# Kernel optimization log

Hardware: AMD Instinct MI355X
Metric: run time of the kernel (lower is better)

The kernel has to match this reference:

```python
import jax, jax.numpy as jnp
import numpy as np

DIM = 320; HEADS = 8; DHEAD = 40; CTX_DIM = 768
INNER = HEADS * DHEAD; FF_INNER = 4 * DIM
B = 1; N = 4096; M = 77
SCALE = DHEAD ** -0.5


def setup_inputs() -> dict:
    key = jax.random.key(0)
    ks = jax.random.split(key, 16)
    p = lambda i, shape: jax.random.normal(ks[i], shape, dtype=jnp.float32) * 0.02
    return {
        "x": jax.random.normal(ks[0], (B, N, DIM), dtype=jnp.float32),
        "context": jax.random.normal(ks[1], (B, M, CTX_DIM), dtype=jnp.float32),
        "focused_attention_mask": jax.random.uniform(ks[2], (1, M, M), dtype=jnp.float32),
        "g1": jnp.ones((DIM,), jnp.float32), "b1": jnp.zeros((DIM,), jnp.float32),
        "g2": jnp.ones((DIM,), jnp.float32), "b2": jnp.zeros((DIM,), jnp.float32),
        "g3": jnp.ones((DIM,), jnp.float32), "b3": jnp.zeros((DIM,), jnp.float32),
        "Wq1": p(3, (DIM, INNER)), "Wk1": p(4, (DIM, INNER)), "Wv1": p(5, (DIM, INNER)),
        "Wo1": p(6, (INNER, DIM)), "bo1": jnp.zeros((DIM,), jnp.float32),
        "Wq2": p(7, (DIM, INNER)), "Wk2": p(8, (CTX_DIM, INNER)), "Wv2": p(9, (CTX_DIM, INNER)),
        "Wo2": p(10, (INNER, DIM)), "bo2": jnp.zeros((DIM,), jnp.float32),
        "Wff1": p(11, (DIM, 2 * FF_INNER)), "bff1": jnp.zeros((2 * FF_INNER,), jnp.float32),
        "Wff2": p(12, (FF_INNER, DIM)), "bff2": jnp.zeros((DIM,), jnp.float32),
        "use_fca": 1,
    }


def _ln(x, g, b):
    mu = x.mean(-1, keepdims=True)
    var = jnp.mean((x - mu) ** 2, -1, keepdims=True)
    return (x - mu) * jax.lax.rsqrt(var + 1e-5) * g + b


def _attn(xn, ctx, Wq, Wk, Wv, Wo, bo, fam, use_fca):
    b, n, _ = xn.shape
    heads = lambda t: t.reshape(b, t.shape[1], HEADS, DHEAD).transpose(0, 2, 1, 3)  # b h n d
    q, k, v = heads(xn @ Wq), heads(ctx @ Wk), heads(ctx @ Wv)
    sim = jnp.einsum('bhid,bhjd->bhij', q, k) * SCALE
    if use_fca:
        m = fam.shape[-1]  # fam: [1, m, m], batch must be 1 (repeat_interleave semantics)
        fw = jnp.einsum('bhqk,dk->bhqd', sim[..., :m], fam[0])
        fw = jnp.minimum(jnp.abs(fw), 1.0)
        fw = fw / (jnp.max(fw, axis=-1, keepdims=True) + 1e-6)
        fw = (fw > 0.6).astype(sim.dtype)
        sim = sim.at[..., :m].add((fw - 1.0) * 50.0)
    a = jax.nn.softmax(sim, axis=-1)
    o = jnp.einsum('bhij,bhjd->bhid', a, v).transpose(0, 2, 1, 3).reshape(b, n, INNER)
    return o @ Wo + bo


def reference(x, context, focused_attention_mask,
              g1, b1, g2, b2, g3, b3,
              Wq1, Wk1, Wv1, Wo1, bo1,
              Wq2, Wk2, Wv2, Wo2, bo2,
              Wff1, bff1, Wff2, bff2, use_fca):
    # attn1: self-attention (context=None in original -> use_fca forced to 0)
    h1 = _ln(x, g1, b1)
    x = _attn(h1, h1, Wq1, Wk1, Wv1, Wo1, bo1, None, 0) + x
    # attn2: cross-attention with focused-attention mask
    h2 = _ln(x, g2, b2)
    x = _attn(h2, context, Wq2, Wk2, Wv2, Wo2, bo2, focused_attention_mask, int(use_fca)) + x
    # GEGLU feed-forward
    h3 = _ln(x, g3, b3)
    proj = h3 @ Wff1 + bff1
    a_, gate = jnp.split(proj, 2, axis=-1)
    x = (a_ * jax.nn.gelu(gate, approximate=False)) @ Wff2 + bff2 + x
    return x
```

## Files before the change

kernel.cpp:

```cpp
#include <hip/hip_runtime.h>
#include <math.h>

typedef __bf16 bf16_t;
typedef __bf16 bf16x8 __attribute__((ext_vector_type(8)));
typedef __bf16 bf16x4 __attribute__((ext_vector_type(4)));
typedef float  f32x4  __attribute__((ext_vector_type(4)));
typedef _Float16 f16_t;
typedef _Float16 f16x4 __attribute__((ext_vector_type(4)));
typedef _Float16 f16x8 __attribute__((ext_vector_type(8)));
typedef __fp16 hf16x2 __attribute__((ext_vector_type(2)));

static constexpr float ATT_SCALE = 0.15811388300841897f;
static constexpr float SC2 = 0.22811031f;
static constexpr float LOG2E = 1.4426950408889634f;

__device__ __forceinline__ bf16_t f2b(float f) {
  unsigned u = __float_as_uint(f);
  u = (u + 0x7fffu + ((u >> 16) & 1u)) >> 16;
  unsigned short s = (unsigned short)u;
  bf16_t r;
  *(unsigned short*)&r = s;
  return r;
}
__device__ __forceinline__ float b2f(bf16_t b) {
  unsigned short s = *(const unsigned short*)&b;
  return __uint_as_float(((unsigned)s) << 16);
}
__device__ __forceinline__ void sto(float v, float* p)  { *p = v; }
__device__ __forceinline__ void sto(float v, bf16_t* p) { *p = f2b(v); }
__device__ __forceinline__ unsigned pkh2(float a, float b) {
  hf16x2 h = __builtin_amdgcn_cvt_pkrtz(a, b);
  return *(unsigned*)&h;
}

__global__ __launch_bounds__(256) void prep_kernel(
    const float* __restrict__ Wq1, const float* __restrict__ Wk1, const float* __restrict__ Wv1,
    const float* __restrict__ Wo1, const float* __restrict__ Wq2,
    const float* __restrict__ Wk2, const float* __restrict__ Wv2, const float* __restrict__ Wo2,
    const float* __restrict__ Wff1, const float* __restrict__ Wff2,
    const float* __restrict__ fam,
    bf16_t* __restrict__ wqkvt, bf16_t* __restrict__ wo1t, float* __restrict__ wkv2t,
    bf16_t* __restrict__ wo2t, bf16_t* __restrict__ wff1t, bf16_t* __restrict__ wff2t,
    bf16_t* __restrict__ wq2th, bf16_t* __restrict__ wq2tl,
    bf16_t* __restrict__ famh, bf16_t* __restrict__ faml)
{
  const int T1 = 960*320;
  const int T2 = T1 + 320*320;
  const int T3 = T2 + 768*640;
  const int T4 = T3 + 320*320;
  const int T5 = T4 + 2560*320;
  const int T6 = T5 + 320*1280;
  const int T7 = T6 + 320*320;
  const int T8 = T7 + 96*96;
  for (int i = blockIdx.x*256 + threadIdx.x; i < T8; i += gridDim.x*256) {
    if (i < T1) {
      int n = i / 320, k = i - n*320;
      float v = (n < 320) ? Wq1[k*320+n] * SC2
              : (n < 640) ? Wk1[k*320+n-320] : Wv1[k*320+n-640];
      wqkvt[i] = f2b(v);
    } else if (i < T2) {
      int e = i - T1; int n = e / 320, k = e - n*320;
      wo1t[e] = f2b(Wo1[k*320+n]);
    } else if (i < T3) {
      int e = i - T2; int n = e / 768, k = e - n*768;
      wkv2t[e] = (n < 320) ? Wk2[k*320+n] : Wv2[k*320+n-320];
    } else if (i < T4) {
      int e = i - T3; int n = e / 320, k = e - n*320;
      wo2t[e] = f2b(Wo2[k*320+n]);
    } else if (i < T5) {
      int e = i - T4; int n = e / 320, k = e - n*320;
      wff1t[e] = f2b(Wff1[(size_t)k*2560+n]);
    } else if (i < T6) {
      int e = i - T5; int n = e / 1280, k = e - n*1280;
      wff2t[e] = f2b(Wff2[k*320+n]);
    } else if (i < T7) {
      int e = i - T6; int n = e / 320, k = e - n*320;
      float v = Wq2[k*320+n];
      bf16_t h = f2b(v);
      wq2th[e] = h;
      wq2tl[e] = f2b(v - b2f(h));
    } else {
      int e = i - T7; int d = e / 96, k = e - d*96;
      float v = (d < 77 && k < 77) ? fam[d*77 + k] : 0.f;
      bf16_t h = f2b(v);
      famh[e] = h;
      faml[e] = f2b(v - b2f(h));
    }
  }
}

template<typename OT>
__global__ __launch_bounds__(256) void ln_kernel(
    const float* __restrict__ x, const float* __restrict__ g, const float* __restrict__ b,
    OT* __restrict__ out)
{
  const int lane = threadIdx.x & 63;
  const int row = blockIdx.x * 4 + (threadIdx.x >> 6);
  const float* xr = x + (size_t)row * 320;
  float v[5], s = 0.f, s2 = 0.f;
#pragma unroll
  for (int i = 0; i < 5; i++) { v[i] = xr[lane + i*64]; s += v[i]; s2 += v[i]*v[i]; }
#pragma unroll
  for (int o = 32; o; o >>= 1) { s += __shfl_xor(s, o); s2 += __shfl_xor(s2, o); }
  float mu = s * (1.f/320.f);
  float rs = rsqrtf(fmaxf(s2*(1.f/320.f) - mu*mu, 0.f) + 1e-5f);
#pragma unroll
  for (int i = 0; i < 5; i++) {
    int c = lane + i*64;
    sto((v[i]-mu)*rs*g[c] + b[c], &out[(size_t)row*320 + c]);
  }
}

__global__ __launch_bounds__(256) void ln2_split_kernel(
    const float* __restrict__ x, const float* __restrict__ g, const float* __restrict__ b,
    bf16_t* __restrict__ hi, bf16_t* __restrict__ lo)
{
  const int lane = threadIdx.x & 63;
  const int row = blockIdx.x * 4 + (threadIdx.x >> 6);
  const float* xr = x + (size_t)row * 320;
  float v[5], s = 0.f, s2 = 0.f;
#pragma unroll
  for (int i = 0; i < 5; i++) { v[i] = xr[lane + i*64]; s += v[i]; s2 += v[i]*v[i]; }
#pragma unroll
  for (int o = 32; o; o >>= 1) { s += __shfl_xor(s, o); s2 += __shfl_xor(s2, o); }
  float mu = s * (1.f/320.f);
  float rs = rsqrtf(fmaxf(s2*(1.f/320.f) - mu*mu, 0.f) + 1e-5f);
#pragma unroll
  for (int i = 0; i < 5; i++) {
    int c = lane + i*64;
    float y = (v[i]-mu)*rs*g[c] + b[c];
    bf16_t h = f2b(y);
    hi[(size_t)row*320 + c] = h;
    lo[(size_t)row*320 + c] = f2b(y - b2f(h));
  }
}

__global__ __launch_bounds__(256) void kv2_dot_kernel(
    const float* __restrict__ ctx, const float* __restrict__ wkv2t, float* __restrict__ kv2)
{
  const int gid = blockIdx.x*16 + (threadIdx.x >> 4);
  const int q = threadIdx.x & 15;
  const int m = gid / 640, n = gid - m*640;
  const float4* a = (const float4*)(ctx + (size_t)m*768);
  const float4* b = (const float4*)(wkv2t + (size_t)n*768);
  float acc = 0.f;
#pragma unroll
  for (int i = 0; i < 12; i++) {
    float4 av = a[i*16+q], bv = b[i*16+q];
    acc += av.x*bv.x + av.y*bv.y + av.z*bv.z + av.w*bv.w;
  }
#pragma unroll
  for (int o = 8; o; o >>= 1) acc += __shfl_xor(acc, o);
  if (q == 0) kv2[(size_t)m*640 + n] = acc;
}

__global__ __launch_bounds__(256) void kv2_post_kernel(
    const float* __restrict__ kv2, bf16_t* __restrict__ k2h, bf16_t* __restrict__ k2l,
    bf16_t* __restrict__ v2t)
{
  const int NK = 8*96*64;
  const int NV = 8*48*96;
  int i = blockIdx.x*256 + threadIdx.x;
  if (i < NK) {
    int h = i / (96*64), r = i - h*96*64, j = r >> 6, d = r & 63;
    float v = (j < 77 && d < 40) ? kv2[(size_t)j*640 + h*40 + d] : 0.f;
    bf16_t hh = f2b(v);
    k2h[i] = hh;
    k2l[i] = f2b(v - b2f(hh));
  } else if (i < NK + NV) {
    int e = i - NK;
    int h = e / (48*96), r = e - h*48*96, d = r / 96, j = r - d*96;
    v2t[e] = f2b((d < 40 && j < 77) ? kv2[(size_t)j*640 + 320 + h*40 + d] : 0.f);
  }
}

__global__ __launch_bounds__(256) void repack_vt_kernel(
    const bf16_t* __restrict__ qkvb, f16_t* __restrict__ vpack, bf16_t* __restrict__ kpack)
{
  __shared__ f16_t T[64*44];
  const int tid = threadIdx.x;
  const int t0 = blockIdx.x * 64, h = blockIdx.y;
  for (int e = tid; e < 320; e += 256) {
    int t = e / 5, c8 = (e - t*5) * 8;
    bf16x8 v = *(const bf16x8*)(qkvb + (size_t)(t0+t)*960 + 640 + h*40 + c8);
    f16_t* dst = &T[t*44 + c8];
#pragma unroll
    for (int j = 0; j < 8; j++) dst[j] = (f16_t)b2f(v[j]);
  }
  __syncthreads();
  for (int e = tid; e < 3072; e += 256) {
    int dt = e >> 10;
    int r  = e & 1023;
    int g2 = r >> 9, o = r & 511;
    int lane = o >> 3, j = o & 7;
    int qd = lane >> 4, ln = lane & 15;
    int d = dt*16 + ln;
    int key = g2*32 + ((j & 4) ? 16 : 0) + qd*4 + (j & 3);
    float val;
    if (d < 40)       val = (float)T[key*44 + d];
    else if (d == 40) val = 1.0f;
    else              val = 0.0f;
    vpack[(((size_t)h*3 + dt)*128 + (t0 >> 5) + g2)*512 + o] = (f16_t)val;
  }
  for (int e = tid; e < 2560; e += 256) {
    int g = e / 640, o = e - g*640;
    int key = t0 + g*16;
    bf16_t val;
    if (o < 512) {
      int lane = o >> 3, j = o & 7;
      int qd = lane >> 4, ln = lane & 15;
      val = qkvb[(size_t)(key + ln)*960 + 320 + h*40 + qd*8 + j];
    } else {
      int o2 = o - 512; int ln = o2 >> 3, j = o2 & 7;
      val = qkvb[(size_t)(key + ln)*960 + 320 + h*40 + 32 + j];
    }
    kpack[((size_t)h*256 + (t0 >> 4) + g)*640 + o] = val;
  }
}

__global__ __launch_bounds__(256, 4) void flash_self_kernel(
    const bf16_t* __restrict__ qkvb, const bf16_t* __restrict__ kpack,
    const f16_t* __restrict__ vpack,
    float* __restrict__ opart, float* __restrict__ lpart)
{
  __shared__ float Red[6144];
  const int tid = threadIdx.x;
  const int w = tid >> 6, lane = tid & 63;
  const int ln = lane & 15, qd = lane >> 4;
  const int qh = w >> 1, kh = w & 1;
  const int h = blockIdx.x & 7;
  const int q0 = (blockIdx.x >> 3) * 64;
  const int split = blockIdx.y;

  const int kgbase = h*256 + kh*2;
  const int vgbase = h*384 + kh;
  const int lko = lane*8;

  bf16x8 zero8 = {};
  bf16x8 bq[2][2];
#pragma unroll
  for (int nt = 0; nt < 2; nt++) {
    const bf16_t* qp = qkvb + (size_t)(q0 + qh*32 + nt*16 + ln)*960 + h*40;
    bq[nt][0] = *(const bf16x8*)(qp + qd*8);
    bq[nt][1] = (qd == 0) ? *(const bf16x8*)(qp + 32) : zero8;
  }

  f32x4 zero4 = {0.f,0.f,0.f,0.f};
  f32x4 oacc[3][2];
#pragma unroll
  for (int a = 0; a < 3; a++)
#pragma unroll
    for (int b = 0; b < 2; b++) oacc[a][b] = zero4;

#define FS_LOADK(DST, K0)                                                       \
  {                                                                             \
    const bf16_t* kp_ = kpack + ((size_t)kgbase + ((K0) >> 4)) * 640;           \
    DST[0][0] = *(const bf16x8*)(kp_ + lko);                                    \
    DST[0][1] = (qd == 0) ? *(const bf16x8*)(kp_ + 512 + ln*8) : zero8;         \
    DST[1][0] = *(const bf16x8*)(kp_ + 640 + lko);                              \
    DST[1][1] = (qd == 0) ? *(const bf16x8*)(kp_ + 1152 + ln*8) : zero8;        \
  }

#define FS_LOADV(DST, K0)                                                       \
  {                                                                             \
    _Pragma("unroll")                                                           \
    for (int dt_ = 0; dt_ < 3; dt_++)                                           \
      DST[dt_] = *(const f16x8*)(vpack + ((size_t)vgbase + dt_*128 + ((K0) >> 5)) * 512 + lko); \
  }

#define FS_COMPUTE(KA, VA)                                                      \
  {                                                                             \
    _Pragma("unroll")                                                           \
    for (int nt = 0; nt < 2; nt++) {                                            \
      f32x4 s0 = __builtin_amdgcn_mfma_f32_16x16x32_bf16(KA[0][0], bq[nt][0], zero4, 0,0,0); \
      s0 = __builtin_amdgcn_mfma_f32_16x16x32_bf16(KA[0][1], bq[nt][1], s0, 0,0,0); \
      f32x4 s1 = __builtin_amdgcn_mfma_f32_16x16x32_bf16(KA[1][0], bq[nt][0], zero4, 0,0,0); \
      s1 = __builtin_amdgcn_mfma_f32_16x16x32_bf16(KA[1][1], bq[nt][1], s1, 0,0,0); \
      uint4 u_;                                                                 \
      u_.x = pkh2(__builtin_amdgcn_exp2f(s0[0]), __builtin_amdgcn_exp2f(s0[1])); \
      u_.y = pkh2(__builtin_amdgcn_exp2f(s0[2]), __builtin_amdgcn_exp2f(s0[3])); \
      u_.z = pkh2(__builtin_amdgcn_exp2f(s1[0]), __builtin_amdgcn_exp2f(s1[1])); \
      u_.w = pkh2(__builtin_amdgcn_exp2f(s1[2]), __builtin_amdgcn_exp2f(s1[3])); \
      f16x8 pb = *(f16x8*)&u_;                                                  \
      _Pragma("unroll")                                                         \
      for (int dt = 0; dt < 3; dt++)                                            \
        oacc[dt][nt] = __builtin_amdgcn_mfma_f32_16x16x32_f16(VA[dt], pb, oacc[dt][nt], 0,0,0); \
    }                                                                           \
  }

  bf16x8 ka[2][2], kb[2][2];
  f16x8 va[3], vb[3];
  FS_LOADK(ka, split*2048);
#pragma unroll 1
  for (int kt = 0; kt < 32; kt += 2) {
    const int k0 = split*2048 + kt*64;
    FS_LOADV(va, k0);
    FS_LOADK(kb, k0 + 64);
    FS_COMPUTE(ka, va);
    FS_LOADV(vb, k0 + 64);
    FS_LOADK(ka, (kt + 2 < 32) ? (k0 + 128) : split*2048);
    FS_COMPUTE(kb, vb);
  }
#undef FS_LOADK
#undef FS_LOADV
#undef FS_COMPUTE

#pragma unroll
  for (int nt = 0; nt < 2; nt++)
#pragma unroll
    for (int dt = 0; dt < 3; dt++)
      *(f32x4*)&Red[((w*2 + nt)*3 + dt)*256 + ln*16 + qd*4] = oacc[dt][nt];
  __syncthreads();
  float* obase = opart + ((size_t)(split*8 + h)*4096 + q0)*40;
  const int qh2 = tid >> 7, lq = (tid >> 3) & 15, dbase = tid & 7;
#pragma unroll
  for (int nt = 0; nt < 2; nt++) {
#pragma unroll
    for (int i = 0; i < 5; i++) {
      int d = dbase + i*8;
      int dt = d >> 4, dr = d & 15;
      float v = Red[(((qh2*2 + 0)*2 + nt)*3 + dt)*256 + lq*16 + dr]
              + Red[(((qh2*2 + 1)*2 + nt)*3 + dt)*256 + lq*16 + dr];
      obase[(size_t)(qh2*32 + nt*16 + lq)*40 + d] = v;
    }
    if (dbase == 0) {
      float l = Red[(((qh2*2 + 0)*2 + nt)*3 + 2)*256 + lq*16 + 8]
              + Red[(((qh2*2 + 1)*2 + nt)*3 + 2)*256 + lq*16 + 8];
      lpart[(size_t)(split*8 + h)*4096 + q0 + qh2*32 + nt*16 + lq] = l;
    }
  }
}

__global__ __launch_bounds__(256) void merge_o1_kernel(
    const float* __restrict__ op, const float* __restrict__ lp, bf16_t* __restrict__ o1a)
{
  int i = blockIdx.x*256 + threadIdx.x;
  int q = i / 320, c = i - q*320;
  int h = c / 40, d = c - h*40;
  size_t base = ((size_t)h*4096 + q)*40 + d;
  float l = lp[h*4096 + q] + lp[32768 + h*4096 + q];
  float o = op[base] + op[base + 1310720];
  o1a[i] = f2b(o / l);
}

__global__ __launch_bounds__(256) void attn_cross_kernel(
    const float* __restrict__ q2, const bf16_t* __restrict__ k2h, const bf16_t* __restrict__ k2l,
    const bf16_t* __restrict__ famh, const bf16_t* __restrict__ faml,
    const bf16_t* __restrict__ v2t, const int* __restrict__ use_fca,
    bf16_t* __restrict__ o2)
{
  __shared__ bf16_t SMh[4][16*96];
  __shared__ bf16_t SMl[4][16*96];
  __shared__ bf16_t PAs[4][16*96];
  const int tid = threadIdx.x;
  const int w = tid >> 6, lane = tid & 63;
  const int ln = lane & 15, qd = lane >> 4;
  const int h = blockIdx.x & 7;
  const int q0 = (blockIdx.x >> 3)*64 + w*16;
  const int fca = use_fca[0];
  bf16_t* smh = SMh[w];
  bf16_t* sml = SMl[w];
  bf16_t* pa  = PAs[w];

  {
    bf16x4 z = {};
    int q = lane >> 2, c = 80 + (lane & 3)*4;
    *(bf16x4*)&smh[q*96 + c] = z;
    *(bf16x4*)&sml[q*96 + c] = z;
    *(bf16x4*)&pa [q*96 + c] = z;
  }

  bf16x8 zero8 = {};
  bf16x8 aqh0, aql0, aqh1 = zero8, aql1 = zero8;
  {
    const float* qp = q2 + (size_t)(q0 + ln)*320 + h*40;
    float4 v0 = *(const float4*)(qp + qd*8);
    float4 v1 = *(const float4*)(qp + qd*8 + 4);
    float qv[8] = {v0.x,v0.y,v0.z,v0.w,v1.x,v1.y,v1.z,v1.w};
#pragma unroll
    for (int i = 0; i < 8; i++) {
      bf16_t hh = f2b(qv[i]);
      aqh0[i] = hh; aql0[i] = f2b(qv[i] - b2f(hh));
    }
    if (qd == 0) {
      float4 u0 = *(const float4*)(qp + 32);
      float4 u1 = *(const float4*)(qp + 36);
      float uv[8] = {u0.x,u0.y,u0.z,u0.w,u1.x,u1.y,u1.z,u1.w};
#pragma unroll
      for (int i = 0; i < 8; i++) {
        bf16_t hh = f2b(uv[i]);
        aqh1[i] = hh; aql1[i] = f2b(uv[i] - b2f(hh));
      }
    }
  }

  f32x4 zero4 = {0.f,0.f,0.f,0.f};
  float ss[5][4];
#pragma unroll
  for (int nt = 0; nt < 5; nt++) {
    const bf16_t* kb = k2h + ((size_t)h*96 + nt*16 + ln)*64 + qd*8;
    const bf16_t* kl = k2l + ((size_t)h*96 + nt*16 + ln)*64 + qd*8;
    bf16x8 kh0 = *(const bf16x8*)kb;
    bf16x8 kh1 = *(const bf16x8*)(kb + 32);
    bf16x8 kl0 = *(const bf16x8*)kl;
    bf16x8 kl1 = *(const bf16x8*)(kl + 32);
    f32x4 s;
    s = __builtin_amdgcn_mfma_f32_16x16x32_bf16(aqh0, kl0, zero4, 0, 0, 0);
    s = __builtin_amdgcn_mfma_f32_16x16x32_bf16(aql0, kh0, s, 0, 0, 0);
    s = __builtin_amdgcn_mfma_f32_16x16x32_bf16(aqh0, kh0, s, 0, 0, 0);
    s = __builtin_amdgcn_mfma_f32_16x16x32_bf16(aqh1, kl1, s, 0, 0, 0);
    s = __builtin_amdgcn_mfma_f32_16x16x32_bf16(aql1, kh1, s, 0, 0, 0);
    s = __builtin_amdgcn_mfma_f32_16x16x32_bf16(aqh1, kh1, s, 0, 0, 0);
#pragma unroll
    for (int r = 0; r < 4; r++) {
      float sv = s[r] * ATT_SCALE;
      ss[nt][r] = sv;
      bf16_t hh = f2b(sv);
      smh[(qd*4 + r)*96 + nt*16 + ln] = hh;
      sml[(qd*4 + r)*96 + nt*16 + ln] = f2b(sv - b2f(hh));
    }
  }

  f32x4 facc[5];
#pragma unroll
  for (int nt = 0; nt < 5; nt++) facc[nt] = zero4;
#pragma unroll
  for (int c = 0; c < 3; c++) {
    bf16x8 sah = *(const bf16x8*)&smh[ln*96 + c*32 + qd*8];
    bf16x8 sal = *(const bf16x8*)&sml[ln*96 + c*32 + qd*8];
#pragma unroll
    for (int nt = 0; nt < 5; nt++) {
      bf16x8 fh8 = *(const bf16x8*)(famh + ((size_t)(nt*16 + ln))*96 + c*32 + qd*8);
      bf16x8 fl8 = *(const bf16x8*)(faml + ((size_t)(nt*16 + ln))*96 + c*32 + qd*8);
      facc[nt] = __builtin_amdgcn_mfma_f32_16x16x32_bf16(sah, fl8, facc[nt], 0, 0, 0);
      facc[nt] = __builtin_amdgcn_mfma_f32_16x16x32_bf16(sal, fh8, facc[nt], 0, 0, 0);
      facc[nt] = __builtin_amdgcn_mfma_f32_16x16x32_bf16(sah, fh8, facc[nt], 0, 0, 0);
    }
  }

  float pr[5][4];
  if (fca) {
    float fwv[5][4], fm[4];
#pragma unroll
    for (int nt = 0; nt < 5; nt++)
#pragma unroll
      for (int r = 0; r < 4; r++) fwv[nt][r] = fminf(fabsf(facc[nt][r]), 1.f);
#pragma unroll
    for (int r = 0; r < 4; r++) {
      float m = fmaxf(fmaxf(fwv[0][r], fwv[1][r]), fmaxf(fwv[2][r], fmaxf(fwv[3][r], fwv[4][r])));
#pragma unroll
      for (int o = 8; o; o >>= 1) m = fmaxf(m, __shfl_xor(m, o));
      fm[r] = m;
    }
#pragma unroll
    for (int nt = 0; nt < 5; nt++)
#pragma unroll
      for (int r = 0; r < 4; r++) {
        float lg = ss[nt][r] - ((fwv[nt][r] > 0.6f*(fm[r] + 1e-6f)) ? 0.f : 50.f);
        pr[nt][r] = __builtin_amdgcn_exp2f(lg * LOG2E);
      }
  } else {
#pragma unroll
    for (int nt = 0; nt < 5; nt++)
#pragma unroll
      for (int r = 0; r < 4; r++)
        pr[nt][r] = __builtin_amdgcn_exp2f(ss[nt][r] * LOG2E);
  }
  if (ln >= 13) {
#pragma unroll
    for (int r = 0; r < 4; r++) pr[4][r] = 0.f;
  }
  float l_[4] = {0.f,0.f,0.f,0.f};
#pragma unroll
  for (int nt = 0; nt < 5; nt++)
#pragma unroll
    for (int r = 0; r < 4; r++) {
      l_[r] += pr[nt][r];
      pa[(qd*4 + r)*96 + nt*16 + ln] = f2b(pr[nt][r]);
    }
#pragma unroll
  for (int r = 0; r < 4; r++)
#pragma unroll
    for (int o = 8; o; o >>= 1) l_[r] += __shfl_xor(l_[r], o);

  f32x4 oacc[3];
#pragma unroll
  for (int nt = 0; nt < 3; nt++) oacc[nt] = zero4;
#pragma unroll
  for (int c = 0; c < 3; c++) {
    bf16x8 paf = *(const bf16x8*)&pa[ln*96 + c*32 + qd*8];
#pragma unroll
    for (int nt = 0; nt < 3; nt++) {
      bf16x8 vb = *(const bf16x8*)(v2t + ((size_t)h*48 + nt*16 + ln)*96 + c*32 + qd*8);
      oacc[nt] = __builtin_amdgcn_mfma_f32_16x16x32_bf16(paf, vb, oacc[nt], 0, 0, 0);
    }
  }
  float inv[4];
#pragma unroll
  for (int r = 0; r < 4; r++) inv[r] = 1.f / l_[r];
#pragma unroll
  for (int nt = 0; nt < 3; nt++) {
    int d = nt*16 + ln;
    if (d < 40) {
#pragma unroll
      for (int r = 0; r < 4; r++)
        o2[(size_t)(q0 + qd*4 + r)*320 + h*40 + d] = f2b(oacc[nt][r]*inv[r]);
    }
  }
}

template<int OUT_BF16>
__global__ __launch_bounds__(256) void gemm_bf16_kernel(
    const bf16_t* __restrict__ A, const bf16_t* __restrict__ Bt,
    const float* __restrict__ bias, const float* __restrict__ resid,
    void* __restrict__ Cout, int M, int N, int K)
{
  __shared__ bf16_t As[128][72];
  __shared__ bf16_t Bs[64][72];
  const int tid = threadIdx.x;
  const int m0 = blockIdx.x * 128, n0 = blockIdx.y * 64;
  const int w = tid >> 6, lane = tid & 63;
  const int wr = w >> 1, wc = w & 1;
  const int ln = lane & 15, qd = lane >> 4;
  f32x4 zero = {0.f, 0.f, 0.f, 0.f};
  f32x4 acc[4][2];
#pragma unroll
  for (int a = 0; a < 4; a++)
#pragma unroll
    for (int b = 0; b < 2; b++) acc[a][b] = zero;

  for (int k0 = 0; k0 < K; k0 += 64) {
    __syncthreads();
#pragma unroll
    for (int i = 0; i < 4; i++) {
      int vid = tid + i*256;
      int r = vid >> 3, c8 = (vid & 7) * 8;
      *(bf16x8*)&As[r][c8] = *(const bf16x8*)(A + (size_t)(m0+r)*K + k0 + c8);
    }
#pragma unroll
    for (int i = 0; i < 2; i++) {
      int vid = tid + i*256;
      int r = vid >> 3, c8 = (vid & 7) * 8;
      *(bf16x8*)&Bs[r][c8] = *(const bf16x8*)(Bt + (size_t)(n0+r)*K + k0 + c8);
    }
    __syncthreads();
#pragma unroll
    for (int c = 0; c < 2; c++) {
      bf16x8 af[4], bfr[2];
#pragma unroll
      for (int mt = 0; mt < 4; mt++)
        af[mt] = *(const bf16x8*)&As[wr*64 + mt*16 + ln][c*32 + qd*8];
#pragma unroll
      for (int nt = 0; nt < 2; nt++)
        bfr[nt] = *(const bf16x8*)&Bs[wc*32 + nt*16 + ln][c*32 + qd*8];
#pragma unroll
      for (int mt = 0; mt < 4; mt++)
#pragma unroll
        for (int nt = 0; nt < 2; nt++)
          acc[mt][nt] = __builtin_amdgcn_mfma_f32_16x16x32_bf16(af[mt], bfr[nt], acc[mt][nt], 0, 0, 0);
    }
  }
#pragma unroll
  for (int mt = 0; mt < 4; mt++)
#pragma unroll
    for (int nt = 0; nt < 2; nt++)
#pragma unroll
      for (int r = 0; r < 4; r++) {
        int gm = m0 + wr*64 + mt*16 + qd*4 + r;
        int gn = n0 + wc*32 + nt*16 + ln;
        float v = acc[mt][nt][r];
        if (bias)  v += bias[gn];
        if (resid) v += resid[(size_t)gm*N + gn];
        if (OUT_BF16) sto(v, &((bf16_t*)Cout)[(size_t)gm*N + gn]);
        else          sto(v, &((float*)Cout)[(size_t)gm*N + gn]);
      }
}

template<int OUT_BF16>
__global__ __launch_bounds__(256) void gemm_bf16_32_kernel(
    const bf16_t* __restrict__ A, const bf16_t* __restrict__ Bt,
    const float* __restrict__ bias, const float* __restrict__ resid,
    void* __restrict__ Cout, int M, int N, int K)
{
  __shared__ bf16_t As[32][72];
  __shared__ bf16_t Bs[64][72];
  const int tid = threadIdx.x;
  const int m0 = blockIdx.x * 32, n0 = blockIdx.y * 64;
  const int w = tid >> 6, lane = tid & 63;
  const int wr = w >> 1, wc = w & 1;
  const int ln = lane & 15, qd = lane >> 4;
  f32x4 zero = {0.f, 0.f, 0.f, 0.f};
  f32x4 acc[2];
  acc[0] = zero; acc[1] = zero;

  for (int k0 = 0; k0 < K; k0 += 64) {
    __syncthreads();
    {
      int r = tid >> 3, c8 = (tid & 7) * 8;
      *(bf16x8*)&As[r][c8] = *(const bf16x8*)(A + (size_t)(m0+r)*K + k0 + c8);
    }
#pragma unroll
    for (int i = 0; i < 2; i++) {
      int vid = tid + i*256;
      int r = vid >> 3, c8 = (vid & 7) * 8;
      *(bf16x8*)&Bs[r][c8] = *(const bf16x8*)(Bt + (size_t)(n0+r)*K + k0 + c8);
    }
    __syncthreads();
#pragma unroll
    for (int c = 0; c < 2; c++) {
      bf16x8 af = *(const bf16x8*)&As[wr*16 + ln][c*32 + qd*8];
#pragma unroll
      for (int nt = 0; nt < 2; nt++) {
        bf16x8 bfr = *(const bf16x8*)&Bs[wc*32 + nt*16 + ln][c*32 + qd*8];
        acc[nt] = __builtin_amdgcn_mfma_f32_16x16x32_bf16(af, bfr, acc[nt], 0, 0, 0);
      }
    }
  }
#pragma unroll
  for (int nt = 0; nt < 2; nt++)
#pragma unroll
    for (int r = 0; r < 4; r++) {
      int gm = m0 + wr*16 + qd*4 + r;
      int gn = n0 + wc*32 + nt*16 + ln;
      float v = acc[nt][r];
      if (bias)  v += bias[gn];
      if (resid) v += resid[(size_t)gm*N + gn];
      if (OUT_BF16) sto(v, &((bf16_t*)Cout)[(size_t)gm*N + gn]);
      else          sto(v, &((float*)Cout)[(size_t)gm*N + gn]);
    }
}

__global__ __launch_bounds__(256) void gemm3_32_kernel(
    const bf16_t* __restrict__ Ah, const bf16_t* __restrict__ Al,
    const bf16_t* __restrict__ Bth, const bf16_t* __restrict__ Btl,
    float* __restrict__ C, int M, int N, int K)
{
  __shared__ bf16_t Ash[32][72];
  __shared__ bf16_t Asl[32][72];
  __shared__ bf16_t Bsh[64][72];
  __shared__ bf16_t Bsl[64][72];
  const int tid = threadIdx.x;
  const int m0 = blockIdx.x * 32, n0 = blockIdx.y * 64;
  const int w = tid >> 6, lane = tid & 63;
  const int wr = w >> 1, wc = w & 1;
  const int ln = lane & 15, qd = lane >> 4;
  f32x4 zero = {0.f, 0.f, 0.f, 0.f};
  f32x4 acc[2];
  acc[0] = zero; acc[1] = zero;

  for (int k0 = 0; k0 < K; k0 += 64) {
    __syncthreads();
    {
      int r = tid >> 3, c8 = (tid & 7) * 8;
      *(bf16x8*)&Ash[r][c8] = *(const bf16x8*)(Ah + (size_t)(m0+r)*K + k0 + c8);
      *(bf16x8*)&Asl[r][c8] = *(const bf16x8*)(Al + (size_t)(m0+r)*K + k0 + c8);
    }
#pragma unroll
    for (int i = 0; i < 2; i++) {
      int vid = tid + i*256;
      int r = vid >> 3, c8 = (vid & 7) * 8;
      *(bf16x8*)&Bsh[r][c8] = *(const bf16x8*)(Bth + (size_t)(n0+r)*K + k0 + c8);
      *(bf16x8*)&Bsl[r][c8] = *(const bf16x8*)(Btl + (size_t)(n0+r)*K + k0 + c8);
    }
    __syncthreads();
#pragma unroll
    for (int c = 0; c < 2; c++) {
      bf16x8 afh = *(const bf16x8*)&Ash[wr*16 + ln][c*32 + qd*8];
      bf16x8 afl = *(const bf16x8*)&Asl[wr*16 + ln][c*32 + qd*8];
#pragma unroll
      for (int nt = 0; nt < 2; nt++) {
        bf16x8 bfh = *(const bf16x8*)&Bsh[wc*32 + nt*16 + ln][c*32 + qd*8];
        bf16x8 bfl = *(const bf16x8*)&Bsl[wc*32 + nt*16 + ln][c*32 + qd*8];
        acc[nt] = __builtin_amdgcn_mfma_f32_16x16x32_bf16(afh, bfl, acc[nt], 0, 0, 0);
        acc[nt] = __builtin_amdgcn_mfma_f32_16x16x32_bf16(afl, bfh, acc[nt], 0, 0, 0);
        acc[nt] = __builtin_amdgcn_mfma_f32_16x16x32_bf16(afh, bfh, acc[nt], 0, 0, 0);
      }
    }
  }
#pragma unroll
  for (int nt = 0; nt < 2; nt++)
#pragma unroll
    for (int r = 0; r < 4; r++) {
      int gm = m0 + wr*16 + qd*4 + r;
      int gn = n0 + wc*32 + nt*16 + ln;
      C[(size_t)gm*N + gn] = acc[nt][r];
    }
}

__global__ __launch_bounds__(256) void geglu_kernel(
    const bf16_t* __restrict__ proj, bf16_t* __restrict__ gg)
{
  int idx = blockIdx.x * 256 + threadIdx.x;
  int m = idx / 320, c4 = (idx - m*320) * 4;
  bf16x4 a = *(const bf16x4*)(proj + (size_t)m*2560 + c4);
  bf16x4 g = *(const bf16x4*)(proj + (size_t)m*2560 + 1280 + c4);
  bf16x4 r;
#pragma unroll
  for (int i = 0; i < 4; i++) {
    float gf = b2f(g[i]);
    float ge = 0.5f * gf * (1.f + erff(gf * 0.70710678118654752f));
    r[i] = f2b(b2f(a[i]) * ge);
  }
  *(bf16x4*)(gg + (size_t)m*1280 + c4) = r;
}

extern "C" void kernel_launch(void* const* d_in, const int* in_sizes, int n_in,
                              void* d_out, int out_size, void* d_ws, size_t ws_size,
                              hipStream_t stream)
{
  const float* x    = (const float*)d_in[0];
  const float* ctx  = (const float*)d_in[1];
  const float* fam  = (const float*)d_in[2];
  const float* g1   = (const float*)d_in[3];
  const float* b1   = (const float*)d_in[4];
  const float* g2   = (const float*)d_in[5];
  const float* b2   = (const float*)d_in[6];
  const float* g3   = (const float*)d_in[7];
  const float* b3   = (const float*)d_in[8];
  const float* Wq1  = (const float*)d_in[9];
  const float* Wk1  = (const float*)d_in[10];
  const float* Wv1  = (const float*)d_in[11];
  const float* Wo1  = (const float*)d_in[12];
  const float* bo1  = (const float*)d_in[13];
  const float* Wq2  = (const float*)d_in[14];
  const float* Wk2  = (const float*)d_in[15];
  const float* Wv2  = (const float*)d_in[16];
  const float* Wo2  = (const float*)d_in[17];
  const float* bo2  = (const float*)d_in[18];
  const float* Wff1 = (const float*)d_in[19];
  const float* bff1 = (const float*)d_in[20];
  const float* Wff2 = (const float*)d_in[21];
  const float* bff2 = (const float*)d_in[22];
  const int*   ufca = (const int*)d_in[23];

  char* ws = (char*)d_ws;
  bf16_t* qkvb = (bf16_t*)(ws + 0);
  f16_t*  vpack = (f16_t*)(ws + 7864320);
  bf16_t* o1a  = (bf16_t*)(ws + 11010048);
  bf16_t* kpack = (bf16_t*)(ws + 11010048);
  bf16_t* h1b  = (bf16_t*)(ws + 13631488);
  bf16_t* h2hi = (bf16_t*)(ws + 16252928);
  bf16_t* h2lo = (bf16_t*)(ws + 18874368);
  float*  x2   = (float*)(ws + 21495808);
  float*  q2   = (float*)(ws + 26738688);
  float*  kv2  = (float*)(ws + 31981568);
  bf16_t* o2   = (bf16_t*)(ws + 32178688);
  float*  x3   = (float*)(ws + 34800128);
  bf16_t* h3b  = (bf16_t*)(ws + 40043008);
  bf16_t* wqkvt = (bf16_t*)(ws + 42664448);
  bf16_t* wo1t  = (bf16_t*)(ws + 43278848);
  float*  wkv2t = (float*)(ws + 43483648);
  bf16_t* wo2t  = (bf16_t*)(ws + 45449728);
  bf16_t* wff1t = (bf16_t*)(ws + 45654528);
  bf16_t* wff2t = (bf16_t*)(ws + 47292928);
  float*  lpart = (float*)(ws + 48112128);
  bf16_t* wq2th = (bf16_t*)(ws + 48374272);
  bf16_t* wq2tl = (bf16_t*)(ws + 48579072);
  bf16_t* famh  = (bf16_t*)(ws + 48783872);
  bf16_t* faml  = (bf16_t*)(ws + 48802304);
  bf16_t* k2h   = (bf16_t*)(ws + 48820736);
  bf16_t* k2l   = (bf16_t*)(ws + 48919040);
  bf16_t* v2t   = (bf16_t*)(ws + 49017344);
  float*  opart = (float*)(ws + 21495808);
  bf16_t* proj = (bf16_t*)(ws + 0);
  bf16_t* gg   = (bf16_t*)(ws + 21495808);

  float* xout = (float*)d_out;

  prep_kernel<<<2048, 256, 0, stream>>>(Wq1, Wk1, Wv1, Wo1, Wq2, Wk2, Wv2, Wo2, Wff1, Wff2, fam,
                                        wqkvt, wo1t, wkv2t, wo2t, wff1t, wff2t, wq2th, wq2tl,
                                        famh, faml);
  ln_kernel<bf16_t><<<1024, 256, 0, stream>>>(x, g1, b1, h1b);
  gemm_bf16_kernel<1><<<dim3(32,15), 256, 0, stream>>>(h1b, wqkvt, nullptr, nullptr, qkvb, 4096, 960, 320);
  repack_vt_kernel<<<dim3(64,8), 256, 0, stream>>>(qkvb, vpack, kpack);
  flash_self_kernel<<<dim3(512,2), 256, 0, stream>>>(qkvb, kpack, vpack, opart, lpart);
  merge_o1_kernel<<<5120, 256, 0, stream>>>(opart, lpart, o1a);
  gemm_bf16_32_kernel<0><<<dim3(128,5), 256, 0, stream>>>(o1a, wo1t, bo1, x, x2, 4096, 320, 320);
  ln2_split_kernel<<<1024, 256, 0, stream>>>(x2, g2, b2, h2hi, h2lo);
  gemm3_32_kernel<<<dim3(128,5), 256, 0, stream>>>(h2hi, h2lo, wq2th, wq2tl, q2, 4096, 320, 320);
  kv2_dot_kernel<<<3080, 256, 0, stream>>>(ctx, wkv2t, kv2);
  kv2_post_kernel<<<336, 256, 0, stream>>>(kv2, k2h, k2l, v2t);
  attn_cross_kernel<<<512, 256, 0, stream>>>(q2, k2h, k2l, famh, faml, v2t, ufca, o2);
  gemm_bf16_32_kernel<0><<<dim3(128,5), 256, 0, stream>>>(o2, wo2t, bo2, x2, x3, 4096, 320, 320);
  ln_kernel<bf16_t><<<1024, 256, 0, stream>>>(x3, g3, b3, h3b);
  gemm_bf16_kernel<1><<<dim3(32,40), 256, 0, stream>>>(h3b, wff1t, bff1, nullptr, proj, 4096, 2560, 320);
  geglu_kernel<<<5120, 256, 0, stream>>>(proj, gg);
  gemm_bf16_32_kernel<0><<<dim3(128,5), 256, 0, stream>>>(gg, wff2t, bff2, x3, xout, 4096, 320, 1280);
}
```

Measured before the change: 284.0 us.

## Fuse GEGLU into FF1 GEMM, fuse kv2 post-processing, enlarge GEMM row tiles

New measurement: 302.2 us. 1.06x slower.

```diff
diff --git a/kernel.cpp b/kernel.cpp
--- a/kernel.cpp
+++ b/kernel.cpp
@@ -42,7 +42,8 @@
     bf16_t* __restrict__ wqkvt, bf16_t* __restrict__ wo1t, float* __restrict__ wkv2t,
     bf16_t* __restrict__ wo2t, bf16_t* __restrict__ wff1t, bf16_t* __restrict__ wff2t,
     bf16_t* __restrict__ wq2th, bf16_t* __restrict__ wq2tl,
-    bf16_t* __restrict__ famh, bf16_t* __restrict__ faml)
+    bf16_t* __restrict__ famh, bf16_t* __restrict__ faml,
+    bf16_t* __restrict__ zpad)
 {
   const int T1 = 960*320;
   const int T2 = T1 + 320*320;
@@ -52,7 +53,8 @@
   const int T6 = T5 + 320*1280;
   const int T7 = T6 + 320*320;
   const int T8 = T7 + 96*96;
-  for (int i = blockIdx.x*256 + threadIdx.x; i < T8; i += gridDim.x*256) {
+  const int T9 = T8 + 135168;
+  for (int i = blockIdx.x*256 + threadIdx.x; i < T9; i += gridDim.x*256) {
     if (i < T1) {
       int n = i / 320, k = i - n*320;
       float v = (n < 320) ? Wq1[k*320+n] * SC2
@@ -79,12 +81,14 @@
       bf16_t h = f2b(v);
       wq2th[e] = h;
       wq2tl[e] = f2b(v - b2f(h));
-    } else {
+    } else if (i < T8) {
       int e = i - T7; int d = e / 96, k = e - d*96;
       float v = (d < 77 && k < 77) ? fam[d*77 + k] : 0.f;
       bf16_t h = f2b(v);
       famh[e] = h;
       faml[e] = f2b(v - b2f(h));
+    } else {
+      zpad[i - T8] = f2b(0.f);
     }
   }
 }
@@ -136,7 +140,8 @@
 }
 
 __global__ __launch_bounds__(256) void kv2_dot_kernel(
-    const float* __restrict__ ctx, const float* __restrict__ wkv2t, float* __restrict__ kv2)
+    const float* __restrict__ ctx, const float* __restrict__ wkv2t,
+    bf16_t* __restrict__ k2h, bf16_t* __restrict__ k2l, bf16_t* __restrict__ v2t)
 {
   const int gid = blockIdx.x*16 + (threadIdx.x >> 4);
   const int q = threadIdx.x & 15;
@@ -151,26 +156,17 @@
   }
 #pragma unroll
   for (int o = 8; o; o >>= 1) acc += __shfl_xor(acc, o);
-  if (q == 0) kv2[(size_t)m*640 + n] = acc;
-}
-
-__global__ __launch_bounds__(256) void kv2_post_kernel(
-    const float* __restrict__ kv2, bf16_t* __restrict__ k2h, bf16_t* __restrict__ k2l,
-    bf16_t* __restrict__ v2t)
-{
-  const int NK = 8*96*64;
-  const int NV = 8*48*96;
-  int i = blockIdx.x*256 + threadIdx.x;
-  if (i < NK) {
-    int h = i / (96*64), r = i - h*96*64, j = r >> 6, d = r & 63;
-    float v = (j < 77 && d < 40) ? kv2[(size_t)j*640 + h*40 + d] : 0.f;
-    bf16_t hh = f2b(v);
-    k2h[i] = hh;
-    k2l[i] = f2b(v - b2f(hh));
-  } else if (i < NK + NV) {
-    int e = i - NK;
-    int h = e / (48*96), r = e - h*48*96, d = r / 96, j = r - d*96;
-    v2t[e] = f2b((d < 40 && j < 77) ? kv2[(size_t)j*640 + 320 + h*40 + d] : 0.f);
+  if (q == 0) {
+    if (n < 320) {
+      int h = n / 40, d = n - h*40;
+      int i = h*6144 + m*64 + d;
+      bf16_t hh = f2b(acc);
+      k2h[i] = hh;
+      k2l[i] = f2b(acc - b2f(hh));
+    } else {
+      int n2 = n - 320; int h = n2 / 40, d = n2 - h*40;
+      v2t[h*4608 + d*96 + m] = f2b(acc);
+    }
   }
 }
 
@@ -577,131 +573,203 @@
 }
 
 template<int OUT_BF16>
-__global__ __launch_bounds__(256) void gemm_bf16_32_kernel(
+__global__ __launch_bounds__(256) void gemm_bf16_64_kernel(
     const bf16_t* __restrict__ A, const bf16_t* __restrict__ Bt,
     const float* __restrict__ bias, const float* __restrict__ resid,
     void* __restrict__ Cout, int M, int N, int K)
 {
-  __shared__ bf16_t As[32][72];
+  __shared__ bf16_t As[64][72];
   __shared__ bf16_t Bs[64][72];
   const int tid = threadIdx.x;
-  const int m0 = blockIdx.x * 32, n0 = blockIdx.y * 64;
+  const int m0 = blockIdx.x * 64, n0 = blockIdx.y * 64;
   const int w = tid >> 6, lane = tid & 63;
   const int wr = w >> 1, wc = w & 1;
   const int ln = lane & 15, qd = lane >> 4;
   f32x4 zero = {0.f, 0.f, 0.f, 0.f};
-  f32x4 acc[2];
-  acc[0] = zero; acc[1] = zero;
+  f32x4 acc[2][2];
+#pragma unroll
+  for (int a = 0; a < 2; a++)
+#pragma unroll
+    for (int b = 0; b < 2; b++) acc[a][b] = zero;
 
   for (int k0 = 0; k0 < K; k0 += 64) {
     __syncthreads();
-    {
-      int r = tid >> 3, c8 = (tid & 7) * 8;
-      *(bf16x8*)&As[r][c8] = *(const bf16x8*)(A + (size_t)(m0+r)*K + k0 + c8);
-    }
 #pragma unroll
     for (int i = 0; i < 2; i++) {
       int vid = tid + i*256;
       int r = vid >> 3, c8 = (vid & 7) * 8;
+      *(bf16x8*)&As[r][c8] = *(const bf16x8*)(A + (size_t)(m0+r)*K + k0 + c8);
       *(bf16x8*)&Bs[r][c8] = *(const bf16x8*)(Bt + (size_t)(n0+r)*K + k0 + c8);
     }
     __syncthreads();
 #pragma unroll
     for (int c = 0; c < 2; c++) {
-      bf16x8 af = *(const bf16x8*)&As[wr*16 + ln][c*32 + qd*8];
-#pragma unroll
-      for (int nt = 0; nt < 2; nt++) {
-        bf16x8 bfr = *(const bf16x8*)&Bs[wc*32 + nt*16 + ln][c*32 + qd*8];
-        acc[nt] = __builtin_amdgcn_mfma_f32_16x16x32_bf16(af, bfr, acc[nt], 0, 0, 0);
+      bf16x8 af[2], bfr[2];
+#pragma unroll
+      for (int mt = 0; mt < 2; mt++)
+        af[mt] = *(const bf16x8*)&As[wr*32 + mt*16 + ln][c*32 + qd*8];
+#pragma unroll
+      for (int nt = 0; nt < 2; nt++)
+        bfr[nt] = *(const bf16x8*)&Bs[wc*32 + nt*16 + ln][c*32 + qd*8];
+#pragma unroll
+      for (int mt = 0; mt < 2; mt++)
+#pragma unroll
+        for (int nt = 0; nt < 2; nt++)
+          acc[mt][nt] = __builtin_amdgcn_mfma_f32_16x16x32_bf16(af[mt], bfr[nt], acc[mt][nt], 0, 0, 0);
+    }
+  }
+#pragma unroll
+  for (int mt = 0; mt < 2; mt++)
+#pragma unroll
+    for (int nt = 0; nt < 2; nt++)
+#pragma unroll
+      for (int r = 0; r < 4; r++) {
+        int gm = m0 + wr*32 + mt*16 + qd*4 + r;
+        int gn = n0 + wc*32 + nt*16 + ln;
+        float v = acc[mt][nt][r];
+        if (bias)  v += bias[gn];
+        if (resid) v += resid[(size_t)gm*N + gn];
+        if (OUT_BF16) sto(v, &((bf16_t*)Cout)[(size_t)gm*N + gn]);
+        else          sto(v, &((float*)Cout)[(size_t)gm*N + gn]);
       }
-    }
-  }
-#pragma unroll
-  for (int nt = 0; nt < 2; nt++)
-#pragma unroll
-    for (int r = 0; r < 4; r++) {
-      int gm = m0 + wr*16 + qd*4 + r;
-      int gn = n0 + wc*32 + nt*16 + ln;
-      float v = acc[nt][r];
-      if (bias)  v += bias[gn];
-      if (resid) v += resid[(size_t)gm*N + gn];
-      if (OUT_BF16) sto(v, &((bf16_t*)Cout)[(size_t)gm*N + gn]);
-      else          sto(v, &((float*)Cout)[(size_t)gm*N + gn]);
-    }
-}
-
-__global__ __launch_bounds__(256) void gemm3_32_kernel(
+}
+
+__global__ __launch_bounds__(256) void gemm3_64_kernel(
     const bf16_t* __restrict__ Ah, const bf16_t* __restrict__ Al,
     const bf16_t* __restrict__ Bth, const bf16_t* __restrict__ Btl,
     float* __restrict__ C, int M, int N, int K)
 {
-  __shared__ bf16_t Ash[32][72];
-  __shared__ bf16_t Asl[32][72];
+  __shared__ bf16_t Ash[64][72];
+  __shared__ bf16_t Asl[64][72];
   __shared__ bf16_t Bsh[64][72];
   __shared__ bf16_t Bsl[64][72];
   const int tid = threadIdx.x;
-  const int m0 = blockIdx.x * 32, n0 = blockIdx.y * 64;
+  const int m0 = blockIdx.x * 64, n0 = blockIdx.y * 64;
   const int w = tid >> 6, lane = tid & 63;
   const int wr = w >> 1, wc = w & 1;
   const int ln = lane & 15, qd = lane >> 4;
   f32x4 zero = {0.f, 0.f, 0.f, 0.f};
-  f32x4 acc[2];
-  acc[0] = zero; acc[1] = zero;
+  f32x4 acc[2][2];
+#pragma unroll
+  for (int a = 0; a < 2; a++)
+#pragma unroll
+    for (int b = 0; b < 2; b++) acc[a][b] = zero;
 
   for (int k0 = 0; k0 < K; k0 += 64) {
     __syncthreads();
-    {
-      int r = tid >> 3, c8 = (tid & 7) * 8;
-      *(bf16x8*)&Ash[r][c8] = *(const bf16x8*)(Ah + (size_t)(m0+r)*K + k0 + c8);
-      *(bf16x8*)&Asl[r][c8] = *(const bf16x8*)(Al + (size_t)(m0+r)*K + k0 + c8);
-    }
 #pragma unroll
     for (int i = 0; i < 2; i++) {
       int vid = tid + i*256;
       int r = vid >> 3, c8 = (vid & 7) * 8;
+      *(bf16x8*)&Ash[r][c8] = *(const bf16x8*)(Ah + (size_t)(m0+r)*K + k0 + c8);
+      *(bf16x8*)&Asl[r][c8] = *(const bf16x8*)(Al + (size_t)(m0+r)*K + k0 + c8);
       *(bf16x8*)&Bsh[r][c8] = *(const bf16x8*)(Bth + (size_t)(n0+r)*K + k0 + c8);
       *(bf16x8*)&Bsl[r][c8] = *(const bf16x8*)(Btl + (size_t)(n0+r)*K + k0 + c8);
     }
     __syncthreads();
 #pragma unroll
     for (int c = 0; c < 2; c++) {
-      bf16x8 afh = *(const bf16x8*)&Ash[wr*16 + ln][c*32 + qd*8];
-      bf16x8 afl = *(const bf16x8*)&Asl[wr*16 + ln][c*32 + qd*8];
+      bf16x8 afh[2], afl[2], bfh[2], bfl[2];
+#pragma unroll
+      for (int mt = 0; mt < 2; mt++) {
+        afh[mt] = *(const bf16x8*)&Ash[wr*32 + mt*16 + ln][c*32 + qd*8];
+        afl[mt] = *(const bf16x8*)&Asl[wr*32 + mt*16 + ln][c*32 + qd*8];
+      }
 #pragma unroll
       for (int nt = 0; nt < 2; nt++) {
-        bf16x8 bfh = *(const bf16x8*)&Bsh[wc*32 + nt*16 + ln][c*32 + qd*8];
-        bf16x8 bfl = *(const bf16x8*)&Bsl[wc*32 + nt*16 + ln][c*32 + qd*8];
-        acc[nt] = __builtin_amdgcn_mfma_f32_16x16x32_bf16(afh, bfl, acc[nt], 0, 0, 0);
-        acc[nt] = __builtin_amdgcn_mfma_f32_16x16x32_bf16(afl, bfh, acc[nt], 0, 0, 0);
-        acc[nt] = __builtin_amdgcn_mfma_f32_16x16x32_bf16(afh, bfh, acc[nt], 0, 0, 0);
+        bfh[nt] = *(const bf16x8*)&Bsh[wc*32 + nt*16 + ln][c*32 + qd*8];
+        bfl[nt] = *(const bf16x8*)&Bsl[wc*32 + nt*16 + ln][c*32 + qd*8];
       }
-    }
-  }
-#pragma unroll
-  for (int nt = 0; nt < 2; nt++)
-#pragma unroll
-    for (int r = 0; r < 4; r++) {
-      int gm = m0 + wr*16 + qd*4 + r;
-      int gn = n0 + wc*32 + nt*16 + ln;
-      C[(size_t)gm*N + gn] = acc[nt][r];
-    }
-}
-
-__global__ __launch_bounds__(256) void geglu_kernel(
-    const bf16_t* __restrict__ proj, bf16_t* __restrict__ gg)
-{
-  int idx = blockIdx.x * 256 + threadIdx.x;
-  int m = idx / 320, c4 = (idx - m*320) * 4;
-  bf16x4 a = *(const bf16x4*)(proj + (size_t)m*2560 + c4);
-  bf16x4 g = *(const bf16x4*)(proj + (size_t)m*2560 + 1280 + c4);
-  bf16x4 r;
-#pragma unroll
-  for (int i = 0; i < 4; i++) {
-    float gf = b2f(g[i]);
-    float ge = 0.5f * gf * (1.f + erff(gf * 0.70710678118654752f));
-    r[i] = f2b(b2f(a[i]) * ge);
-  }
-  *(bf16x4*)(gg + (size_t)m*1280 + c4) = r;
+#pragma unroll
+      for (int mt = 0; mt < 2; mt++)
+#pragma unroll
+        for (int nt = 0; nt < 2; nt++) {
+          acc[mt][nt] = __builtin_amdgcn_mfma_f32_16x16x32_bf16(afh[mt], bfl[nt], acc[mt][nt], 0, 0, 0);
+          acc[mt][nt] = __builtin_amdgcn_mfma_f32_16x16x32_bf16(afl[mt], bfh[nt], acc[mt][nt], 0, 0, 0);
+          acc[mt][nt] = __builtin_amdgcn_mfma_f32_16x16x32_bf16(afh[mt], bfh[nt], acc[mt][nt], 0, 0, 0);
+        }
+    }
+  }
+#pragma unroll
+  for (int mt = 0; mt < 2; mt++)
+#pragma unroll
+    for (int nt = 0; nt < 2; nt++)
+#pragma unroll
+      for (int r = 0; r < 4; r++) {
+        int gm = m0 + wr*32 + mt*16 + qd*4 + r;
+        int gn = n0 + wc*32 + nt*16 + ln;
+        C[(size_t)gm*N + gn] = acc[mt][nt][r];
+      }
+}
+
+__global__ __launch_bounds__(256) void gemm_geglu_kernel(
+    const bf16_t* __restrict__ A, const bf16_t* __restrict__ Bt,
+    const float* __restrict__ bias, bf16_t* __restrict__ gg, int K)
+{
+  __shared__ bf16_t As[128][72];
+  __shared__ bf16_t Ba[64][72];
+  __shared__ bf16_t Bg[64][72];
+  const int tid = threadIdx.x;
+  const int m0 = blockIdx.x * 128, n0 = blockIdx.y * 64;
+  const int w = tid >> 6, lane = tid & 63;
+  const int wr = w >> 1, wc = w & 1;
+  const int ln = lane & 15, qd = lane >> 4;
+  f32x4 zero = {0.f, 0.f, 0.f, 0.f};
+  f32x4 acca[4][2], accg[4][2];
+#pragma unroll
+  for (int a = 0; a < 4; a++)
+#pragma unroll
+    for (int b = 0; b < 2; b++) { acca[a][b] = zero; accg[a][b] = zero; }
+
+  for (int k0 = 0; k0 < K; k0 += 64) {
+    __syncthreads();
+#pragma unroll
+    for (int i = 0; i < 4; i++) {
+      int vid = tid + i*256;
+      int r = vid >> 3, c8 = (vid & 7) * 8;
+      *(bf16x8*)&As[r][c8] = *(const bf16x8*)(A + (size_t)(m0+r)*K + k0 + c8);
+    }
+#pragma unroll
+    for (int i = 0; i < 2; i++) {
+      int vid = tid + i*256;
+      int r = vid >> 3, c8 = (vid & 7) * 8;
+      *(bf16x8*)&Ba[r][c8] = *(const bf16x8*)(Bt + (size_t)(n0+r)*K + k0 + c8);
+      *(bf16x8*)&Bg[r][c8] = *(const bf16x8*)(Bt + (size_t)(n0+r+1280)*K + k0 + c8);
+    }
+    __syncthreads();
+#pragma unroll
+    for (int c = 0; c < 2; c++) {
+      bf16x8 af[4], ba[2], bg[2];
+#pragma unroll
+      for (int mt = 0; mt < 4; mt++)
+        af[mt] = *(const bf16x8*)&As[wr*64 + mt*16 + ln][c*32 + qd*8];
+#pragma unroll
+      for (int nt = 0; nt < 2; nt++) {
+        ba[nt] = *(const bf16x8*)&Ba[wc*32 + nt*16 + ln][c*32 + qd*8];
+        bg[nt] = *(const bf16x8*)&Bg[wc*32 + nt*16 + ln][c*32 + qd*8];
+      }
+#pragma unroll
+      for (int mt = 0; mt < 4; mt++)
+#pragma unroll
+        for (int nt = 0; nt < 2; nt++) {
+          acca[mt][nt] = __builtin_amdgcn_mfma_f32_16x16x32_bf16(af[mt], ba[nt], acca[mt][nt], 0, 0, 0);
+          accg[mt][nt] = __builtin_amdgcn_mfma_f32_16x16x32_bf16(af[mt], bg[nt], accg[mt][nt], 0, 0, 0);
+        }
+    }
+  }
+#pragma unroll
+  for (int mt = 0; mt < 4; mt++)
+#pragma unroll
+    for (int nt = 0; nt < 2; nt++)
+#pragma unroll
+      for (int r = 0; r < 4; r++) {
+        int gm = m0 + wr*64 + mt*16 + qd*4 + r;
+        int gn = n0 + wc*32 + nt*16 + ln;
+        float va = acca[mt][nt][r] + bias[gn];
+        float vg = accg[mt][nt][r] + bias[1280 + gn];
+        float ge = 0.5f * vg * (1.f + erff(vg * 0.70710678118654752f));
+        gg[(size_t)gm*1280 + gn] = f2b(va * ge);
+      }
 }
 
 extern "C" void kernel_launch(void* const* d_in, const int* in_sizes, int n_in,
@@ -743,7 +811,6 @@
   bf16_t* h2lo = (bf16_t*)(ws + 18874368);
   float*  x2   = (float*)(ws + 21495808);
   float*  q2   = (float*)(ws + 26738688);
-  float*  kv2  = (float*)(ws + 31981568);
   bf16_t* o2   = (bf16_t*)(ws + 32178688);
   float*  x3   = (float*)(ws + 34800128);
   bf16_t* h3b  = (bf16_t*)(ws + 40043008);
@@ -762,28 +829,25 @@
   bf16_t* k2l   = (bf16_t*)(ws + 48919040);
   bf16_t* v2t   = (bf16_t*)(ws + 49017344);
   float*  opart = (float*)(ws + 21495808);
-  bf16_t* proj = (bf16_t*)(ws + 0);
   bf16_t* gg   = (bf16_t*)(ws + 21495808);
 
   float* xout = (float*)d_out;
 
   prep_kernel<<<2048, 256, 0, stream>>>(Wq1, Wk1, Wv1, Wo1, Wq2, Wk2, Wv2, Wo2, Wff1, Wff2, fam,
                                         wqkvt, wo1t, wkv2t, wo2t, wff1t, wff2t, wq2th, wq2tl,
-                                        famh, faml);
+                                        famh, faml, k2h);
   ln_kernel<bf16_t><<<1024, 256, 0, stream>>>(x, g1, b1, h1b);
   gemm_bf16_kernel<1><<<dim3(32,15), 256, 0, stream>>>(h1b, wqkvt, nullptr, nullptr, qkvb, 4096, 960, 320);
   repack_vt_kernel<<<dim3(64,8), 256, 0, stream>>>(qkvb, vpack, kpack);
   flash_self_kernel<<<dim3(512,2), 256, 0, stream>>>(qkvb, kpack, vpack, opart, lpart);
   merge_o1_kernel<<<5120, 256, 0, stream>>>(opart, lpart, o1a);
-  gemm_bf16_32_kernel<0><<<dim3(128,5), 256, 0, stream>>>(o1a, wo1t, bo1, x, x2, 4096, 320, 320);
+  gemm_bf16_64_kernel<0><<<dim3(64,5), 256, 0, stream>>>(o1a, wo1t, bo1, x, x2, 4096, 320, 320);
   ln2_split_kernel<<<1024, 256, 0, stream>>>(x2, g2, b2, h2hi, h2lo);
-  gemm3_32_kernel<<<dim3(128,5), 256, 0, stream>>>(h2hi, h2lo, wq2th, wq2tl, q2, 4096, 320, 320);
-  kv2_dot_kernel<<<3080, 256, 0, stream>>>(ctx, wkv2t, kv2);
-  kv2_post_kernel<<<336, 256, 0, stream>>>(kv2, k2h, k2l, v2t);
+  gemm3_64_kernel<<<dim3(64,5), 256, 0, stream>>>(h2hi, h2lo, wq2th, wq2tl, q2, 4096, 320, 320);
+  kv2_dot_kernel<<<3080, 256, 0, stream>>>(ctx, wkv2t, k2h, k2l, v2t);
   attn_cross_kernel<<<512, 256, 0, stream>>>(q2, k2h, k2l, famh, faml, v2t, ufca, o2);
-  gemm_bf16_32_kernel<0><<<dim3(128,5), 256, 0, stream>>>(o2, wo2t, bo2, x2, x3, 4096, 320, 320);
+  gemm_bf16_64_kernel<0><<<dim3(64,5), 256, 0, stream>>>(o2, wo2t, bo2, x2, x3, 4096, 320, 320);
   ln_kernel<bf16_t><<<1024, 256, 0, stream>>>(x3, g3, b3, h3b);
-  gemm_bf16_kernel<1><<<dim3(32,40), 256, 0, stream>>>(h3b, wff1t, bff1, nullptr, proj, 4096, 2560, 320);
-  geglu_kernel<<<5120, 256, 0, stream>>>(proj, gg);
-  gemm_bf16_32_kernel<0><<<dim3(128,5), 256, 0, stream>>>(gg, wff2t, bff2, x3, xout, 4096, 320, 1280);
-}
+  gemm_geglu_kernel<<<dim3(32,20), 256, 0, stream>>>(h3b, wff1t, bff1, gg, 320);
+  gemm_bf16_64_kernel<0><<<dim3(64,5), 256, 0, stream>>>(gg, wff2t, bff2, x3, xout, 4096, 320, 1280);
+}
```
